# Performance work log

Measured on AMD Instinct MI355X. Metric: run time of the kernel, lower is better.

The kernel has to match this reference:

```python
import jax, jax.numpy as jnp
import numpy as np

N, ID, OD, M, S, L = 65536, 16, 8, 1024, 8, 64


def setup_inputs() -> dict:
    key = jax.random.key(0)
    k1, k2, k3, k4, k5, k6 = jax.random.split(key, 6)
    return {
        "x": jax.random.normal(k1, (N, ID), dtype=jnp.float32),
        "inducing_locations": jax.random.uniform(k2, (M, ID), dtype=jnp.float32),
        "inducing_weights": jax.random.normal(k3, (S, OD, M), dtype=jnp.float32),
        "prior_frequency": jax.random.normal(k4, (OD, ID, L), dtype=jnp.float32),
        "prior_phase": jax.random.uniform(k5, (OD, L), dtype=jnp.float32, maxval=2 * np.pi),
        "prior_weights": jax.random.normal(k6, (S, OD, L), dtype=jnp.float32),
    }


def _rbf_matrix(x, z):
    # ExponentiatedQuadratic with amplitude=1, length_scale=1:
    # k(x,z) = exp(-0.5 * ||x - z||^2)
    x2 = jnp.sum(x * x, axis=-1)[:, None]          # [N,1]
    z2 = jnp.sum(z * z, axis=-1)[None, :]          # [1,M]
    sq = jnp.maximum(x2 + z2 - 2.0 * (x @ z.T), 0.0)
    return jnp.exp(-0.5 * sq)                      # [N,M]


def reference(x, inducing_locations, inducing_weights, prior_frequency, prior_phase, prior_weights):
    # ---- prior (random Fourier features) ----
    # spectral_weights for unit RBF: outer_weights = ones((OD,L)), inner_weights = ones((ID,))
    # rescaled_x = x / 1 = x
    # basis_fn_inner_prod: [OD, N, L]
    inner = jnp.einsum('ni,oil->onl', x, prior_frequency)
    basis_fn = jnp.cos(inner + prior_phase[:, None, :])              # [OD,N,L]
    basis_weight = jnp.sqrt(2.0 / prior_frequency.shape[-1]) * prior_weights  # [S,OD,L]
    f_prior = jnp.einsum('onl,sol->son', basis_fn, basis_weight)     # [S,OD,N]

    # ---- data term (kernel matrix + matvec) ----
    K = _rbf_matrix(x, inducing_locations)                           # [N,M]
    f_data = jnp.einsum('nm,som->son', K, inducing_weights)          # [S,OD,N]

    return f_prior + f_data
```

## Files before the change

kernel.cpp:

```cpp
#include <hip/hip_runtime.h>
#include <hip/hip_bf16.h>

#define N_PTS 65536
#define LOG2E 1.4426950408889634f
#define INV2PI 0.15915494309189535f

typedef __attribute__((ext_vector_type(8))) short short8;
typedef __attribute__((ext_vector_type(4))) float float4v;
typedef __attribute__((ext_vector_type(4))) unsigned int uint4v;

#if __has_builtin(__builtin_amdgcn_exp2f)
#define EXP2F(x) __builtin_amdgcn_exp2f(x)
#else
#define EXP2F(x) exp2f(x)
#endif

#if __has_builtin(__builtin_amdgcn_cosf) && __has_builtin(__builtin_amdgcn_fractf)
#define COSR(x) __builtin_amdgcn_cosf(__builtin_amdgcn_fractf(x))
#else
#define COSR(x) __cosf((x) * 6.283185307179586f)
#endif

__device__ __forceinline__ short f2b(float f) {
    __hip_bfloat16 h = __float2bfloat16(f);
    return *(short*)&h;
}
__device__ __forceinline__ float b2f(short s) {
    __hip_bfloat16 h = *(__hip_bfloat16*)&s;
    return __bfloat162float(h);
}

__device__ __forceinline__ unsigned int pk2(float a, float b) {
    union { __hip_bfloat162 h; unsigned int u; } cv;
    cv.h = __float22bfloat162_rn(make_float2(a, b));
    return cv.u;
}

__device__ __forceinline__ int permrow(int p) {
    return ((p & 12) << 1) + (p & 3) + ((p >> 4) << 2);
}

__global__ __launch_bounds__(256) void prep_kernel(
    const float* __restrict__ z, const float* __restrict__ W,
    const float* __restrict__ F, const float* __restrict__ pw,
    const float* __restrict__ ph,
    short* __restrict__ zb, short* __restrict__ FbB,
    short* __restrict__ BWd, short* __restrict__ Wtb,
    float* __restrict__ nz2P, float* __restrict__ phP)
{
    int t = blockIdx.x * 256 + threadIdx.x;
    if (t < 16384) {
        int row = t >> 4, i = t & 15;
        int src = (row & ~31) + permrow(row & 31);
        zb[t] = f2b(LOG2E * z[src * 16 + i]);
    } else if (t < 17408) {
        int m = t - 16384;
        int src = (m & ~31) + permrow(m & 31);
        const float4v* zp = (const float4v*)(z + (size_t)src * 16);
        float s = 0.f;
        #pragma unroll
        for (int k = 0; k < 4; k++) {
            float4v v = zp[k];
            float a0 = b2f(f2b(v.x)), a1 = b2f(f2b(v.y));
            float a2 = b2f(f2b(v.z)), a3 = b2f(f2b(v.w));
            s += a0 * a0 + a1 * a1 + a2 * a2 + a3 * a3;
        }
        nz2P[m] = -(0.5f * LOG2E * s);
    } else if (t < 25600) {
        int p = t - 17408;
        int row = p >> 4, i = p & 15;
        int srow = (row & ~31) + permrow(row & 31);
        int o = srow >> 6, l = srow & 63;
        FbB[p] = f2b(INV2PI * F[o * 1024 + i * 64 + l]);
    } else if (t < 58368) {
        int p = t - 25600;
        int so = p >> 9, ol = p & 511, o = ol >> 6;
        float v = ((so & 7) == o) ? 0.17677669529663687f * pw[so * 64 + (ol & 63)] : 0.f;
        BWd[p] = f2b(v);
    } else if (t < 123904) {
        int p = t - 58368;
        Wtb[p] = f2b(W[p]);
    } else {
        int j = t - 123904;
        int sj = (j & ~31) + permrow(j & 31);
        phP[j] = INV2PI * ph[sj];
    }
}

__global__ __launch_bounds__(256, 4) void fused_kernel(
    const float* __restrict__ x,
    const short* __restrict__ zb, const short* __restrict__ FbB,
    const short* __restrict__ BWd, const short* __restrict__ Wtb,
    const float* __restrict__ nz2P, const float* __restrict__ phP,
    float* __restrict__ out)
{
    __shared__ float x2c[64];
    __shared__ __align__(16) float rbufA[64 * 68];
    __shared__ __align__(16) float rbufB[64 * 68];

    const int tid = threadIdx.x;
    const int lane = tid & 63, w = tid >> 6;
    const int q = lane >> 4, c = lane & 15;
    const int n0 = blockIdx.x * 64;

    if (tid < 64) {
        float s = 0.f;
        const float4v* xr = (const float4v*)(x + (size_t)(n0 + tid) * 16);
        #pragma unroll
        for (int k = 0; k < 4; k++) {
            float4v v = xr[k];
            float a0 = b2f(f2b(v.x)), a1 = b2f(f2b(v.y));
            float a2 = b2f(f2b(v.z)), a3 = b2f(f2b(v.w));
            s += a0 * a0 + a1 * a1 + a2 * a2 + a3 * a3;
        }
        x2c[tid] = 0.5f * LOG2E * s;
    }

    short8 ax[4];
    #pragma unroll
    for (int nt = 0; nt < 4; nt++) {
        ax[nt] = (short8)0;
        if (q < 2) {
            const float4v* xp = (const float4v*)(x + (size_t)(n0 + nt * 16 + c) * 16 + q * 8);
            float4v v0 = xp[0], v1 = xp[1];
            ax[nt][0] = f2b(v0.x); ax[nt][1] = f2b(v0.y);
            ax[nt][2] = f2b(v0.z); ax[nt][3] = f2b(v0.w);
            ax[nt][4] = f2b(v1.x); ax[nt][5] = f2b(v1.y);
            ax[nt][6] = f2b(v1.z); ax[nt][7] = f2b(v1.w);
        }
    }

    float4v acc[4][4];
    #pragma unroll
    for (int a = 0; a < 4; a++)
        #pragma unroll
        for (int nt = 0; nt < 4; nt++) acc[a][nt] = (float4v)(0.f);

    __syncthreads();

    const int mbase = w * 256;
    #pragma unroll 2
    for (int mb = 0; mb < 8; mb++) {
        const int m0 = mbase + mb * 32;
        short8 bzA = (short8)0, bzB = (short8)0;
        if (q < 2) {
            bzA = *(const short8*)(zb + (size_t)(m0 + c) * 16 + q * 8);
            bzB = *(const short8*)(zb + (size_t)(m0 + 16 + c) * 16 + q * 8);
        }
        float4v c0A = *(const float4v*)(nz2P + m0 + 4 * q);
        float4v c0B = *(const float4v*)(nz2P + m0 + 16 + 4 * q);
        short8 pb[4];
        #pragma unroll
        for (int nt = 0; nt < 4; nt++) {
            float4v dA = __builtin_amdgcn_mfma_f32_16x16x32_bf16(bzA, ax[nt], c0A, 0, 0, 0);
            float4v dB = __builtin_amdgcn_mfma_f32_16x16x32_bf16(bzB, ax[nt], c0B, 0, 0, 0);
            uint4v u;
            u[0] = pk2(EXP2F(dA[0]), EXP2F(dA[1]));
            u[1] = pk2(EXP2F(dA[2]), EXP2F(dA[3]));
            u[2] = pk2(EXP2F(dB[0]), EXP2F(dB[1]));
            u[3] = pk2(EXP2F(dB[2]), EXP2F(dB[3]));
            pb[nt] = __builtin_bit_cast(short8, u);
        }
        #pragma unroll
        for (int a = 0; a < 4; a++) {
            short8 aw = *(const short8*)(Wtb + (size_t)(a * 16 + c) * 1024 + m0 + q * 8);
            #pragma unroll
            for (int nt = 0; nt < 4; nt++)
                acc[a][nt] = __builtin_amdgcn_mfma_f32_16x16x32_bf16(aw, pb[nt], acc[a][nt], 0, 0, 0);
        }
    }

    #pragma unroll
    for (int nt = 0; nt < 4; nt++) {
        float sxv = EXP2F(-x2c[nt * 16 + c]);
        #pragma unroll
        for (int a = 0; a < 4; a++) acc[a][nt] *= sxv;
    }

    const int lbase = w * 128;
    #pragma unroll 2
    for (int lb = 0; lb < 4; lb++) {
        const int l0 = lbase + lb * 32;
        short8 bfA = (short8)0, bfB = (short8)0;
        if (q < 2) {
            bfA = *(const short8*)(FbB + (size_t)(l0 + c) * 16 + q * 8);
            bfB = *(const short8*)(FbB + (size_t)(l0 + 16 + c) * 16 + q * 8);
        }
        float4v c0A = *(const float4v*)(phP + l0 + 4 * q);
        float4v c0B = *(const float4v*)(phP + l0 + 16 + 4 * q);
        short8 pb[4];
        #pragma unroll
        for (int nt = 0; nt < 4; nt++) {
            float4v dA = __builtin_amdgcn_mfma_f32_16x16x32_bf16(bfA, ax[nt], c0A, 0, 0, 0);
            float4v dB = __builtin_amdgcn_mfma_f32_16x16x32_bf16(bfB, ax[nt], c0B, 0, 0, 0);
            uint4v u;
            u[0] = pk2(COSR(dA[0]), COSR(dA[1]));
            u[1] = pk2(COSR(dA[2]), COSR(dA[3]));
            u[2] = pk2(COSR(dB[0]), COSR(dB[1]));
            u[3] = pk2(COSR(dB[2]), COSR(dB[3]));
            pb[nt] = __builtin_bit_cast(short8, u);
        }
        #pragma unroll
        for (int a = 0; a < 4; a++) {
            short8 aw = *(const short8*)(BWd + (size_t)(a * 16 + c) * 512 + l0 + q * 8);
            #pragma unroll
            for (int nt = 0; nt < 4; nt++)
                acc[a][nt] = __builtin_amdgcn_mfma_f32_16x16x32_bf16(aw, pb[nt], acc[a][nt], 0, 0, 0);
        }
    }

    __syncthreads();
    if (w & 1) {
        float* rb = (w == 1) ? rbufA : rbufB;
        #pragma unroll
        for (int a = 0; a < 4; a++)
            #pragma unroll
            for (int nt = 0; nt < 4; nt++)
                #pragma unroll
                for (int r = 0; r < 4; r++)
                    rb[(a * 16 + 4 * q + r) * 68 + nt * 16 + c] = acc[a][nt][r];
    }
    __syncthreads();
    if (!(w & 1)) {
        float* rb = (w == 0) ? rbufA : rbufB;
        #pragma unroll
        for (int a = 0; a < 4; a++)
            #pragma unroll
            for (int nt = 0; nt < 4; nt++)
                #pragma unroll
                for (int r = 0; r < 4; r++) {
                    int idx = (a * 16 + 4 * q + r) * 68 + nt * 16 + c;
                    rb[idx] += acc[a][nt][r];
                }
    }
    __syncthreads();
    #pragma unroll
    for (int k = 0; k < 16; k++) {
        int idx = k * 256 + tid;
        int row = idx >> 6, nn = idx & 63;
        out[(size_t)row * N_PTS + n0 + nn] = rbufA[row * 68 + nn] + rbufB[row * 68 + nn];
    }
}

extern "C" void kernel_launch(void* const* d_in, const int* in_sizes, int n_in,
                              void* d_out, int out_size, void* d_ws, size_t ws_size,
                              hipStream_t stream) {
    const float* x  = (const float*)d_in[0];
    const float* z  = (const float*)d_in[1];
    const float* W  = (const float*)d_in[2];
    const float* F  = (const float*)d_in[3];
    const float* ph = (const float*)d_in[4];
    const float* pw = (const float*)d_in[5];
    float* out = (float*)d_out;

    char* ws = (char*)d_ws;
    short* zb   = (short*)(ws);
    short* FbB  = (short*)(ws + 32768);
    short* BWd  = (short*)(ws + 49152);
    short* Wtb  = (short*)(ws + 114688);
    float* nz2P = (float*)(ws + 245760);
    float* phP  = (float*)(ws + 249856);

    prep_kernel<<<486, 256, 0, stream>>>(z, W, F, pw, ph, zb, FbB, BWd, Wtb, nz2P, phP);
    fused_kernel<<<1024, 256, 0, stream>>>(x, zb, FbB, BWd, Wtb, nz2P, phP, out);
}
```

Baseline: 115.3 us.

## Use K=16 bf16 MFMA for distance/phase GEMMs and interleave exp with accumulation

The K=16 inner products (x·z and x·F) now use the 16x16x16 bf16 MFMA, so no half-zero-padded 16x16x32 instruction is issued and the q<2 predicated loads go away. The inner loop is restructured: the four weight fragments are loaded up front, and each nt's exp/cos results feed the accumulate MFMAs straight away, with no pb[4] staging array. The goal is to cut wasted MFMA work and let transcendental VALU work overlap the matrix ops. The bf16 packing now uses scalar f2b conversions rather than packed pk2, which may emit more conversion instructions.

```diff
diff --git a/kernel.cpp b/kernel.cpp
--- a/kernel.cpp
+++ b/kernel.cpp
@@ -6,8 +6,8 @@
 #define INV2PI 0.15915494309189535f
 
 typedef __attribute__((ext_vector_type(8))) short short8;
+typedef __attribute__((ext_vector_type(4))) short short4v;
 typedef __attribute__((ext_vector_type(4))) float float4v;
-typedef __attribute__((ext_vector_type(4))) unsigned int uint4v;
 
 #if __has_builtin(__builtin_amdgcn_exp2f)
 #define EXP2F(x) __builtin_amdgcn_exp2f(x)
@@ -30,10 +30,45 @@
     return __bfloat162float(h);
 }
 
-__device__ __forceinline__ unsigned int pk2(float a, float b) {
-    union { __hip_bfloat162 h; unsigned int u; } cv;
-    cv.h = __float22bfloat162_rn(make_float2(a, b));
-    return cv.u;
+#if __has_builtin(__builtin_amdgcn_mfma_f32_16x16x16bf16_1k)
+#define HAVE_MFMA16 1
+typedef short4v pafrag;
+__device__ __forceinline__ float4v pmfma(pafrag a, pafrag b, float4v c) {
+    return __builtin_amdgcn_mfma_f32_16x16x16bf16_1k(a, b, c, 0, 0, 0);
+}
+#else
+#define HAVE_MFMA16 0
+typedef short8 pafrag;
+__device__ __forceinline__ float4v pmfma(pafrag a, pafrag b, float4v c) {
+    return __builtin_amdgcn_mfma_f32_16x16x32_bf16(a, b, c, 0, 0, 0);
+}
+#endif
+
+__device__ __forceinline__ pafrag ldrow(const short* base, int row16, int q, int c) {
+#if HAVE_MFMA16
+    return *(const pafrag*)(base + (size_t)(row16 + c) * 16 + 4 * q);
+#else
+    pafrag v = (pafrag)0;
+    if (q < 2) v = *(const pafrag*)(base + (size_t)(row16 + c) * 16 + 8 * q);
+    return v;
+#endif
+}
+__device__ __forceinline__ pafrag mkxfrag(const float* x, size_t row, int q) {
+#if HAVE_MFMA16
+    float4v v = *(const float4v*)(x + row * 16 + 4 * q);
+    pafrag a;
+    a[0] = f2b(v.x); a[1] = f2b(v.y); a[2] = f2b(v.z); a[3] = f2b(v.w);
+    return a;
+#else
+    pafrag a = (pafrag)0;
+    if (q < 2) {
+        const float4v* xp = (const float4v*)(x + row * 16 + 8 * q);
+        float4v v0 = xp[0], v1 = xp[1];
+        a[0] = f2b(v0.x); a[1] = f2b(v0.y); a[2] = f2b(v0.z); a[3] = f2b(v0.w);
+        a[4] = f2b(v1.x); a[5] = f2b(v1.y); a[6] = f2b(v1.z); a[7] = f2b(v1.w);
+    }
+    return a;
+#endif
 }
 
 __device__ __forceinline__ int permrow(int p) {
@@ -116,19 +151,10 @@
         x2c[tid] = 0.5f * LOG2E * s;
     }
 
-    short8 ax[4];
-    #pragma unroll
-    for (int nt = 0; nt < 4; nt++) {
-        ax[nt] = (short8)0;
-        if (q < 2) {
-            const float4v* xp = (const float4v*)(x + (size_t)(n0 + nt * 16 + c) * 16 + q * 8);
-            float4v v0 = xp[0], v1 = xp[1];
-            ax[nt][0] = f2b(v0.x); ax[nt][1] = f2b(v0.y);
-            ax[nt][2] = f2b(v0.z); ax[nt][3] = f2b(v0.w);
-            ax[nt][4] = f2b(v1.x); ax[nt][5] = f2b(v1.y);
-            ax[nt][6] = f2b(v1.z); ax[nt][7] = f2b(v1.w);
-        }
-    }
+    pafrag ax[4];
+    #pragma unroll
+    for (int nt = 0; nt < 4; nt++)
+        ax[nt] = mkxfrag(x, (size_t)(n0 + nt * 16 + c), q);
 
     float4v acc[4][4];
     #pragma unroll
@@ -142,31 +168,27 @@
     #pragma unroll 2
     for (int mb = 0; mb < 8; mb++) {
         const int m0 = mbase + mb * 32;
-        short8 bzA = (short8)0, bzB = (short8)0;
-        if (q < 2) {
-            bzA = *(const short8*)(zb + (size_t)(m0 + c) * 16 + q * 8);
-            bzB = *(const short8*)(zb + (size_t)(m0 + 16 + c) * 16 + q * 8);
-        }
+        pafrag bzA = ldrow(zb, m0, q, c);
+        pafrag bzB = ldrow(zb, m0 + 16, q, c);
         float4v c0A = *(const float4v*)(nz2P + m0 + 4 * q);
         float4v c0B = *(const float4v*)(nz2P + m0 + 16 + 4 * q);
-        short8 pb[4];
+        short8 aw0 = *(const short8*)(Wtb + (size_t)(0 * 16 + c) * 1024 + m0 + q * 8);
+        short8 aw1 = *(const short8*)(Wtb + (size_t)(1 * 16 + c) * 1024 + m0 + q * 8);
+        short8 aw2 = *(const short8*)(Wtb + (size_t)(2 * 16 + c) * 1024 + m0 + q * 8);
+        short8 aw3 = *(const short8*)(Wtb + (size_t)(3 * 16 + c) * 1024 + m0 + q * 8);
         #pragma unroll
         for (int nt = 0; nt < 4; nt++) {
-            float4v dA = __builtin_amdgcn_mfma_f32_16x16x32_bf16(bzA, ax[nt], c0A, 0, 0, 0);
-            float4v dB = __builtin_amdgcn_mfma_f32_16x16x32_bf16(bzB, ax[nt], c0B, 0, 0, 0);
-            uint4v u;
-            u[0] = pk2(EXP2F(dA[0]), EXP2F(dA[1]));
-            u[1] = pk2(EXP2F(dA[2]), EXP2F(dA[3]));
-            u[2] = pk2(EXP2F(dB[0]), EXP2F(dB[1]));
-            u[3] = pk2(EXP2F(dB[2]), EXP2F(dB[3]));
-            pb[nt] = __builtin_bit_cast(short8, u);
-        }
-        #pragma unroll
-        for (int a = 0; a < 4; a++) {
-            short8 aw = *(const short8*)(Wtb + (size_t)(a * 16 + c) * 1024 + m0 + q * 8);
-            #pragma unroll
-            for (int nt = 0; nt < 4; nt++)
-                acc[a][nt] = __builtin_amdgcn_mfma_f32_16x16x32_bf16(aw, pb[nt], acc[a][nt], 0, 0, 0);
+            float4v dA = pmfma(bzA, ax[nt], c0A);
+            float4v dB = pmfma(bzB, ax[nt], c0B);
+            short8 pb;
+            pb[0] = f2b(EXP2F(dA[0])); pb[1] = f2b(EXP2F(dA[1]));
+            pb[2] = f2b(EXP2F(dA[2])); pb[3] = f2b(EXP2F(dA[3]));
+            pb[4] = f2b(EXP2F(dB[0])); pb[5] = f2b(EXP2F(dB[1]));
+            pb[6] = f2b(EXP2F(dB[2])); pb[7] = f2b(EXP2F(dB[3]));
+            acc[0][nt] = __builtin_amdgcn_mfma_f32_16x16x32_bf16(aw0, pb, acc[0][nt], 0, 0, 0);
+            acc[1][nt] = __builtin_amdgcn_mfma_f32_16x16x32_bf16(aw1, pb, acc[1][nt], 0, 0, 0);
+            acc[2][nt] = __builtin_amdgcn_mfma_f32_16x16x32_bf16(aw2, pb, acc[2][nt], 0, 0, 0);
+            acc[3][nt] = __builtin_amdgcn_mfma_f32_16x16x32_bf16(aw3, pb, acc[3][nt], 0, 0, 0);
         }
     }
 
@@ -181,31 +203,27 @@
     #pragma unroll 2
     for (int lb = 0; lb < 4; lb++) {
         const int l0 = lbase + lb * 32;
-        short8 bfA = (short8)0, bfB = (short8)0;
-        if (q < 2) {
-            bfA = *(const short8*)(FbB + (size_t)(l0 + c) * 16 + q * 8);
-            bfB = *(const short8*)(FbB + (size_t)(l0 + 16 + c) * 16 + q * 8);
-        }
+        pafrag bfA = ldrow(FbB, l0, q, c);
+        pafrag bfB = ldrow(FbB, l0 + 16, q, c);
         float4v c0A = *(const float4v*)(phP + l0 + 4 * q);
         float4v c0B = *(const float4v*)(phP + l0 + 16 + 4 * q);
-        short8 pb[4];
+        short8 aw0 = *(const short8*)(BWd + (size_t)(0 * 16 + c) * 512 + l0 + q * 8);
+        short8 aw1 = *(const short8*)(BWd + (size_t)(1 * 16 + c) * 512 + l0 + q * 8);
+        short8 aw2 = *(const short8*)(BWd + (size_t)(2 * 16 + c) * 512 + l0 + q * 8);
+        short8 aw3 = *(const short8*)(BWd + (size_t)(3 * 16 + c) * 512 + l0 + q * 8);
         #pragma unroll
         for (int nt = 0; nt < 4; nt++) {
-            float4v dA = __builtin_amdgcn_mfma_f32_16x16x32_bf16(bfA, ax[nt], c0A, 0, 0, 0);
-            float4v dB = __builtin_amdgcn_mfma_f32_16x16x32_bf16(bfB, ax[nt], c0B, 0, 0, 0);
-            uint4v u;
-            u[0] = pk2(COSR(dA[0]), COSR(dA[1]));
-            u[1] = pk2(COSR(dA[2]), COSR(dA[3]));
-            u[2] = pk2(COSR(dB[0]), COSR(dB[1]));
-            u[3] = pk2(COSR(dB[2]), COSR(dB[3]));
-            pb[nt] = __builtin_bit_cast(short8, u);
-        }
-        #pragma unroll
-        for (int a = 0; a < 4; a++) {
-            short8 aw = *(const short8*)(BWd + (size_t)(a * 16 + c) * 512 + l0 + q * 8);
-            #pragma unroll
-            for (int nt = 0; nt < 4; nt++)
-                acc[a][nt] = __builtin_amdgcn_mfma_f32_16x16x32_bf16(aw, pb[nt], acc[a][nt], 0, 0, 0);
+            float4v dA = pmfma(bfA, ax[nt], c0A);
+            float4v dB = pmfma(bfB, ax[nt], c0B);
+            short8 pb;
+            pb[0] = f2b(COSR(dA[0])); pb[1] = f2b(COSR(dA[1]));
+            pb[2] = f2b(COSR(dA[2])); pb[3] = f2b(COSR(dA[3]));
+            pb[4] = f2b(COSR(dB[0])); pb[5] = f2b(COSR(dB[1]));
+            pb[6] = f2b(COSR(dB[2])); pb[7] = f2b(COSR(dB[3]));
+            acc[0][nt] = __builtin_amdgcn_mfma_f32_16x16x32_bf16(aw0, pb, acc[0][nt], 0, 0, 0);
+            acc[1][nt] = __builtin_amdgcn_mfma_f32_16x16x32_bf16(aw1, pb, acc[1][nt], 0, 0, 0);
+            acc[2][nt] = __builtin_amdgcn_mfma_f32_16x16x32_bf16(aw2, pb, acc[2][nt], 0, 0, 0);
+            acc[3][nt] = __builtin_amdgcn_mfma_f32_16x16x32_bf16(aw3, pb, acc[3][nt], 0, 0, 0);
         }
     }
 
```

Measured after the change: 107.5 us, median of 2. 6.8% less time.
